# Optimization experiments

Measured on AMD Instinct MI355X. Metric: run time of the kernel, lower is better.

The kernel has to match this reference:

```python
import jax, jax.numpy as jnp
import numpy as np

D = 512      # d_model
H = 8        # n_head
NL = 3       # encoder layers
FF = 2048    # torch TransformerEncoderLayer default dim_feedforward
HID = 256    # hidden_size
ACT = 12     # action_size
NOBJ = 89    # num_objects
BAND = 17    # tril(diagonal=-17) -> keys older than 16 steps banned


def setup_inputs() -> dict:
    key = jax.random.key(0)
    ks = iter(jax.random.split(key, 48))
    rn = lambda shape, s=0.02: jax.random.normal(next(ks), shape, jnp.float32) * s
    b, seq = 16, 512
    inp = {
        'state_input': jax.random.normal(next(ks), (b, seq, 3, 16, 16), jnp.float32),
        'goal_input': jax.random.normal(next(ks), (b, seq, 300), jnp.float32),
        # encoders (stand-ins for obs_enc / lang_enc)
        'W_obs': rn((256, 3 * 16 * 16)), 'b_obs': rn((256,)),
        'W_lang': rn((256, 300)), 'b_lang': rn((256,)),
        # input projection 512 -> 512
        'W_in': rn((D, 512)), 'b_in': rn((D,)),
        # per-layer transformer params, stacked on layer dim
        'Wqkv': rn((NL, 3 * D, D)), 'bqkv': rn((NL, 3 * D)),
        'Wo': rn((NL, D, D)), 'bo': rn((NL, D)),
        'W1': rn((NL, FF, D)), 'b1': rn((NL, FF)),
        'W2': rn((NL, D, FF)), 'b2': rn((NL, D)),
        'g1': jnp.ones((NL, D)), 'bt1': jnp.zeros((NL, D)),
        'g2': jnp.ones((NL, D)), 'bt2': jnp.zeros((NL, D)),
        # output heads
        'W_outp': rn((HID, D)), 'b_outp': rn((HID,)),
        'W_a1': rn((ACT, HID)), 'b_a1': rn((ACT,)),
        'W_a2': rn((NOBJ, HID)), 'b_a2': rn((NOBJ,)),
    }
    return inp


def _ln(y, g, bt):
    m = y.mean(-1, keepdims=True)
    v = y.var(-1, keepdims=True)
    return (y - m) / jnp.sqrt(v + 1e-5) * g + bt


def _encoder(x, mask_add, Wqkv, bqkv, Wo, bo, W1, b1, W2, b2, g1, bt1, g2, bt2):
    b, n, _ = x.shape
    dh = D // H
    scale = 1.0 / np.sqrt(dh)
    for l in range(NL):
        qkv = x @ Wqkv[l].T + bqkv[l]
        q, k, v = jnp.split(qkv, 3, axis=-1)
        hd = lambda t: t.reshape(b, n, H, dh).transpose(0, 2, 1, 3)  # [b,h,n,dh]
        q, k, v = hd(q), hd(k), hd(v)
        sc = jnp.einsum('bhqd,bhkd->bhqk', q, k) * scale + mask_add
        a = jax.nn.softmax(sc, axis=-1)
        o = jnp.einsum('bhqk,bhkd->bhqd', a, v).transpose(0, 2, 1, 3).reshape(b, n, D)
        o = o @ Wo[l].T + bo[l]
        x = _ln(x + o, g1[l], bt1[l])             # post-LN (torch default)
        f = jax.nn.relu(x @ W1[l].T + b1[l]) @ W2[l].T + b2[l]
        x = _ln(x + f, g2[l], bt2[l])
    return x


def reference(state_input, goal_input, W_obs, b_obs, W_lang, b_lang, W_in, b_in,
              Wqkv, bqkv, Wo, bo, W1, b1, W2, b2, g1, bt1, g2, bt2,
              W_outp, b_outp, W_a1, b_a1, W_a2, b_a2):
    b, s = state_input.shape[:2]
    st = state_input.reshape(b, s, -1) @ W_obs.T + b_obs          # obs_enc
    lg = goal_input @ W_lang.T + b_lang                            # lang_enc
    x = jnp.concatenate([st, lg], axis=-1) @ W_in.T + b_in        # [b,s,D]
    # key padding mask; sentinel token appended (causal_mask=False branch)
    pad = ~jnp.any(goal_input != -1, axis=-1)                      # [b,s]
    pad = jnp.concatenate([pad, jnp.zeros((b, 1), bool)], axis=1)
    x = jnp.concatenate([x, jnp.zeros((b, 1, D), x.dtype)], axis=1)
    n = s + 1
    i = jnp.arange(n)
    # banned: tril(-17) | triu(1)  -> attend only to keys in [i-16, i]
    mask2 = ((i[:, None] - i[None, :]) >= BAND) | (i[None, :] > i[:, None])
    banned = mask2[None, None, :, :] | pad[:, None, None, :]
    mask_add = jnp.where(banned, jnp.float32(-1e9), jnp.float32(0.0))
    x = _encoder(x, mask_add, Wqkv, bqkv, Wo, bo, W1, b1, W2, b2, g1, bt1, g2, bt2)
    out = x[:, :-1, :]                                             # drop sentinel
    h = out @ W_outp.T + b_outp
    l1 = h @ W_a1.T + b_a1
    l2 = h @ W_a2.T + b_a2
    return jnp.concatenate([l1, l2], axis=-1)                      # [b,s,101]
```

## Files before the change

kernel.cpp:

```cpp
#include <hip/hip_runtime.h>

#define D 512
#define H 8
#define NL 3
#define FFD 2048
#define HID 256
#define BAND 17
#define BATCH 16
#define SEQ 512
#define MTOK (BATCH * SEQ)
#define NOUT 101
#define NOUTP 128

typedef unsigned short u16;
typedef __attribute__((ext_vector_type(8))) short short8;
typedef __attribute__((ext_vector_type(4))) float f32x4;
typedef __attribute__((ext_vector_type(8))) unsigned short u16x8;

__device__ inline float bf2f(u16 u) {
    union { unsigned int i; float f; } x; x.i = ((unsigned int)u) << 16; return x.f;
}
__device__ inline u16 f2bf(float f) {
    union { float f; unsigned int i; } x; x.f = f;
    unsigned int r = x.i + 0x7fffu + ((x.i >> 16) & 1u);
    return (u16)(r >> 16);
}

__device__ __forceinline__ void gload_lds16(const u16* g, u16* l) {
    __builtin_amdgcn_global_load_lds(
        (const __attribute__((address_space(1))) unsigned int*)(g),
        (__attribute__((address_space(3))) unsigned int*)(l),
        16, 0, 0);
}

#define BM 128
#define BN 128
#define BK 64

__global__ __launch_bounds__(512) void gemm_kernel(
    const u16* __restrict__ A, int lda,
    const u16* __restrict__ B, int ldb,
    const float* __restrict__ bias,
    float* __restrict__ Cf, int ldcf,
    u16* __restrict__ Cb0, u16* __restrict__ Cb1, int ldcb,
    int M, int N, int K, int relu)
{
    __shared__ u16 As[2][BM * BK];
    __shared__ u16 Bs[2][BN * BK];
    const int tid  = threadIdx.x;
    const int lane = tid & 63;
    const int wv   = tid >> 6;
    const int wr = wv >> 2, wc = wv & 3;

    const int nb  = gridDim.x * gridDim.y;
    const int bid = blockIdx.y * gridDim.x + blockIdx.x;
    const int tile = (bid & 7) * (nb >> 3) + (bid >> 3);
    const int m0 = (tile / gridDim.x) * BM;
    const int n0 = (tile % gridDim.x) * BN;
    const int kz = blockIdx.z * K;

    f32x4 acc[4][2] = {};

    const int srow8 = lane >> 3;
    const int schunk = (lane & 7) ^ srow8;
    const size_t aoff0 = (size_t)(m0 + wv * 16 + srow8) * lda + kz + schunk * 8;
    const size_t aoff1 = aoff0 + 8 * lda;
    const size_t boff0 = (size_t)(n0 + wv * 16 + srow8) * ldb + kz + schunk * 8;
    const size_t boff1 = boff0 + 8 * ldb;

    const int frow = lane & 15;
    const int q    = lane >> 4;
    const int rc0 = ((q ^ (frow & 7)) << 3);
    const int rc1 = (((4 + q) ^ (frow & 7)) << 3);

    #define STAGE(buf, k0)                                                    \
        do {                                                                  \
            gload_lds16(A + aoff0 + (k0), &As[buf][(wv * 16 + 0) * BK]);      \
            gload_lds16(A + aoff1 + (k0), &As[buf][(wv * 16 + 8) * BK]);      \
            gload_lds16(B + boff0 + (k0), &Bs[buf][(wv * 16 + 0) * BK]);      \
            gload_lds16(B + boff1 + (k0), &Bs[buf][(wv * 16 + 8) * BK]);      \
        } while (0)

    #define COMPUTE(buf)                                                            \
        do {                                                                        \
            short8 af[4][2], bf[2][2];                                              \
            _Pragma("unroll")                                                       \
            for (int i = 0; i < 4; ++i) {                                           \
                const u16* rp = &As[buf][(wr * 64 + i * 16 + frow) * BK];           \
                af[i][0] = *(const short8*)&rp[rc0];                                \
                af[i][1] = *(const short8*)&rp[rc1];                                \
            }                                                                       \
            _Pragma("unroll")                                                       \
            for (int j = 0; j < 2; ++j) {                                           \
                const u16* rp = &Bs[buf][(wc * 32 + j * 16 + frow) * BK];           \
                bf[j][0] = *(const short8*)&rp[rc0];                                \
                bf[j][1] = *(const short8*)&rp[rc1];                                \
            }                                                                       \
            _Pragma("unroll")                                                       \
            for (int kk = 0; kk < 2; ++kk)                                          \
                _Pragma("unroll")                                                   \
                for (int i = 0; i < 4; ++i)                                         \
                    _Pragma("unroll")                                               \
                    for (int j = 0; j < 2; ++j)                                     \
                        acc[i][j] = __builtin_amdgcn_mfma_f32_16x16x32_bf16(        \
                            af[i][kk], bf[j][kk], acc[i][j], 0, 0, 0);              \
        } while (0)

    const int nt = K >> 6;
    STAGE(0, 0);
    int cur = 0;
    for (int t = 0; t < nt - 1; ++t) {
        STAGE(cur ^ 1, (t + 1) << 6);
        asm volatile("s_waitcnt vmcnt(4)" ::: "memory");
        __builtin_amdgcn_s_barrier();
        __builtin_amdgcn_sched_barrier(0);
        COMPUTE(cur);
        __builtin_amdgcn_s_barrier();
        cur ^= 1;
    }
    asm volatile("s_waitcnt vmcnt(0)" ::: "memory");
    __builtin_amdgcn_s_barrier();
    __builtin_amdgcn_sched_barrier(0);
    COMPUTE(cur);

    #undef STAGE
    #undef COMPUTE

    u16* Cb = blockIdx.z ? Cb1 : Cb0;
    const bool addb = (bias != nullptr) && (blockIdx.z == 0);

    const int crow0 = (lane >> 4) * 4;
    const int ccol  = lane & 15;
    #pragma unroll
    for (int j = 0; j < 2; ++j) {
        int gcol = n0 + wc * 32 + j * 16 + ccol;
        if (gcol >= N) continue;
        float bv = addb ? bias[gcol] : 0.f;
        #pragma unroll
        for (int i = 0; i < 4; ++i) {
            #pragma unroll
            for (int r = 0; r < 4; ++r) {
                int grow = m0 + wr * 64 + i * 16 + crow0 + r;
                float v = acc[i][j][r] + bv;
                if (relu) v = fmaxf(v, 0.f);
                if (Cf) Cf[(size_t)grow * ldcf + gcol] = v;
                if (Cb) Cb[(size_t)grow * ldcb + gcol] = f2bf(v);
            }
        }
    }
}

#define CHUNK 128
#define KSLOT 144
#define VT_LD 152

__global__ __launch_bounds__(512) void attn_kernel(
    const u16* __restrict__ qkv, const unsigned char* __restrict__ pad,
    u16* __restrict__ o)
{
    __shared__ u16 Vt[64 * VT_LD];
    __shared__ u16 Pl[8 * 16 * 40];
    __shared__ unsigned char padl[KSLOT];

    const int tid = threadIdx.x, lane = tid & 63, wv = tid >> 6;
    const int b = blockIdx.z, h = blockIdx.y, c0 = blockIdx.x * CHUNK;
    const u16* base = qkv + (size_t)b * SEQ * (3 * D);

    for (int s = tid; s < KSLOT * 4; s += 512) {
        int t = s >> 2, dq = (s & 3) * 16;
        int j = c0 - 16 + t; if (j < 0) j = 0;
        const u16* vrow = base + (size_t)j * (3 * D) + 2 * D + h * 64 + dq;
        u16 tmp[16];
        *(u16x8*)&tmp[0] = *(const u16x8*)&vrow[0];
        *(u16x8*)&tmp[8] = *(const u16x8*)&vrow[8];
        #pragma unroll
        for (int d = 0; d < 16; ++d)
            Vt[(dq + d) * VT_LD + t] = tmp[d];
    }
    if (tid < KSLOT) {
        int j = c0 - 16 + tid;
        padl[tid] = (j >= 0) ? pad[b * SEQ + j] : (unsigned char)1;
    }
    __syncthreads();

    const int qi0 = wv * 16;
    const int i0  = c0 + qi0;
    const int frow = lane & 15;
    const int g    = lane >> 4;
    const int kg8  = g * 8;
    const int g4   = g * 4;

    short8 qf[2];
    #pragma unroll
    for (int kk = 0; kk < 2; ++kk)
        qf[kk] = *(const short8*)&base[(size_t)(i0 + frow) * (3 * D) + h * 64 + kk * 32 + kg8];

    f32x4 sacc[2] = {};
    #pragma unroll
    for (int jb = 0; jb < 2; ++jb) {
        int jrow = i0 - 16 + jb * 16 + frow; if (jrow < 0) jrow = 0;
        const u16* kbase = base + (size_t)jrow * (3 * D) + D + h * 64;
        #pragma unroll
        for (int kk = 0; kk < 2; ++kk) {
            short8 kf = *(const short8*)&kbase[kk * 32 + kg8];
            sacc[jb] = __builtin_amdgcn_mfma_f32_16x16x32_bf16(qf[kk], kf, sacc[jb], 0, 0, 0);
        }
    }

    float sv[2][4];
    #pragma unroll
    for (int jb = 0; jb < 2; ++jb) {
        int s = jb * 16 + frow;
        int jg = i0 - 16 + s;
        bool padk = (jg < 0) || padl[qi0 + s];
        #pragma unroll
        for (int r = 0; r < 4; ++r) {
            int qq = g4 + r;
            bool banned = (s < qq) || (s > qq + 16) || padk;
            sv[jb][r] = sacc[jb][r] * 0.125f + (banned ? -1e9f : 0.f);
        }
    }

    float ex[2][4], rdn[4];
    #pragma unroll
    for (int r = 0; r < 4; ++r) {
        float m = fmaxf(sv[0][r], sv[1][r]);
        #pragma unroll
        for (int off = 1; off < 16; off <<= 1) m = fmaxf(m, __shfl_xor(m, off));
        float e0 = __expf(sv[0][r] - m);
        float e1 = __expf(sv[1][r] - m);
        float dsum = e0 + e1;
        #pragma unroll
        for (int off = 1; off < 16; off <<= 1) dsum += __shfl_xor(dsum, off);
        ex[0][r] = e0; ex[1][r] = e1;
        rdn[r] = 1.f / dsum;
    }

    u16* Pw = &Pl[wv * 640];
    #pragma unroll
    for (int jb = 0; jb < 2; ++jb)
        #pragma unroll
        for (int r = 0; r < 4; ++r)
            Pw[(g4 + r) * 40 + jb * 16 + frow] = f2bf(ex[jb][r]);
    short8 pa = *(const short8*)&Pw[frow * 40 + kg8];

    f32x4 oacc[4] = {};
    #pragma unroll
    for (int nb = 0; nb < 4; ++nb) {
        short8 vf = *(const short8*)&Vt[(nb * 16 + frow) * VT_LD + qi0 + kg8];
        oacc[nb] = __builtin_amdgcn_mfma_f32_16x16x32_bf16(pa, vf, oacc[nb], 0, 0, 0);
    }

    #pragma unroll
    for (int r = 0; r < 4; ++r) {
        size_t row = (size_t)(b * SEQ + i0 + g4 + r);
        #pragma unroll
        for (int nb = 0; nb < 4; ++nb)
            o[row * D + h * 64 + nb * 16 + frow] = f2bf(oacc[nb][r] * rdn[r]);
    }
}

__global__ __launch_bounds__(256) void resln_kernel(
    const u16* __restrict__ xin,
    const u16* __restrict__ d0, const u16* __restrict__ d1,
    const float* __restrict__ g, const float* __restrict__ bt,
    u16* __restrict__ xb)
{
    int row  = blockIdx.x * 4 + (threadIdx.x >> 6);
    int lane = threadIdx.x & 63;
    u16x8 xv = *(const u16x8*)(xin + (size_t)row * D + lane * 8);
    u16x8 dv0 = *(const u16x8*)(d0 + (size_t)row * D + lane * 8);
    u16x8 dv1 = *(const u16x8*)(d1 + (size_t)row * D + lane * 8);

    float y[8];
    float s = 0.f, s2 = 0.f;
    #pragma unroll
    for (int c = 0; c < 8; ++c) {
        y[c] = bf2f(xv[c]) + bf2f(dv0[c]) + bf2f(dv1[c]);
        s += y[c]; s2 += y[c] * y[c];
    }
    #pragma unroll
    for (int off = 32; off > 0; off >>= 1) {
        s  += __shfl_xor(s, off);
        s2 += __shfl_xor(s2, off);
    }
    float mean = s * (1.f / D);
    float var  = s2 * (1.f / D) - mean * mean;
    float inv  = rsqrtf(fmaxf(var, 0.f) + 1e-5f);

    f32x4 gv0 = ((const f32x4*)g)[lane * 2],  gv1 = ((const f32x4*)g)[lane * 2 + 1];
    f32x4 bv0 = ((const f32x4*)bt)[lane * 2], bv1 = ((const f32x4*)bt)[lane * 2 + 1];
    u16x8 ob;
    #pragma unroll
    for (int c = 0; c < 4; ++c) {
        ob[c]     = f2bf((y[c] - mean) * inv * gv0[c] + bv0[c]);
        ob[c + 4] = f2bf((y[c + 4] - mean) * inv * gv1[c] + bv1[c]);
    }
    *(u16x8*)(xb + (size_t)row * D + lane * 8) = ob;
}

__global__ __launch_bounds__(256) void pad_kernel(
    const float* __restrict__ goal, unsigned char* __restrict__ pad)
{
    int row  = blockIdx.x * 4 + (threadIdx.x >> 6);
    int lane = threadIdx.x & 63;
    const f32x4* gr = (const f32x4*)(goal + (size_t)row * 300);
    bool any = false;
    for (int c4 = lane; c4 < 75; c4 += 64) {
        f32x4 v = gr[c4];
        any |= (v[0] != -1.f) | (v[1] != -1.f) | (v[2] != -1.f) | (v[3] != -1.f);
    }
    unsigned long long b = __ballot(any);
    if (lane == 0) pad[row] = (b == 0ull) ? 1 : 0;
}

struct CvtJob { const float* src; u16* dstb; float* dstf; int n; int mode; };
struct CvtArgs { CvtJob j[15]; int blk0[16]; };

__global__ __launch_bounds__(256) void cvt_kernel(CvtArgs a) {
    const int bx = blockIdx.x;
    int jid = 0;
    #pragma unroll 1
    while (jid < 14 && bx >= a.blk0[jid + 1]) ++jid;
    const CvtJob jb = a.j[jid];
    const int i0 = (bx - a.blk0[jid]) * 2048 + threadIdx.x * 8;
    if (i0 >= jb.n) return;

    if (jb.mode == 0) {
        if (i0 + 8 <= jb.n) {
            f32x4 v0 = *(const f32x4*)(jb.src + i0);
            f32x4 v1 = *(const f32x4*)(jb.src + i0 + 4);
            u16x8 o;
            #pragma unroll
            for (int c = 0; c < 4; ++c) { o[c] = f2bf(v0[c]); o[c + 4] = f2bf(v1[c]); }
            *(u16x8*)(jb.dstb + i0) = o;
        } else {
            for (int e = 0; e < 8 && i0 + e < jb.n; ++e) jb.dstb[i0 + e] = f2bf(jb.src[i0 + e]);
        }
    } else if (jb.mode == 2) {
        int r = (int)((unsigned)i0 / 320u);
        int c = i0 - r * 320;
        const float* s = jb.src + (size_t)r * 300 + c;
        u16x8 o;
        if (c + 8 <= 300) {
            f32x4 v0 = *(const f32x4*)s;
            f32x4 v1 = *(const f32x4*)(s + 4);
            #pragma unroll
            for (int cc = 0; cc < 4; ++cc) { o[cc] = f2bf(v0[cc]); o[cc + 4] = f2bf(v1[cc]); }
        } else {
            #pragma unroll
            for (int e = 0; e < 8; ++e) o[e] = (c + e < 300) ? f2bf(s[e]) : (u16)0;
        }
        *(u16x8*)(jb.dstb + i0) = o;
    } else if (jb.mode == 1) {
        for (int e = 0; e < 8 && i0 + e < jb.n; ++e) jb.dstf[i0 + e] = jb.src[i0 + e];
    } else {
        u16x8 z = {0, 0, 0, 0, 0, 0, 0, 0};
        *(u16x8*)(jb.dstb + i0) = z;
    }
}


extern "C" void kernel_launch(void* const* d_in, const int* in_sizes, int n_in,
                              void* d_out, int out_size, void* d_ws, size_t ws_size,
                              hipStream_t stream)
{
    const float* state  = (const float*)d_in[0];
    const float* goal   = (const float*)d_in[1];
    const float* W_obs  = (const float*)d_in[2];
    const float* b_obs  = (const float*)d_in[3];
    const float* W_lang = (const float*)d_in[4];
    const float* b_lang = (const float*)d_in[5];
    const float* W_in   = (const float*)d_in[6];
    const float* b_in   = (const float*)d_in[7];
    const float* Wqkv   = (const float*)d_in[8];
    const float* bqkv   = (const float*)d_in[9];
    const float* Wo     = (const float*)d_in[10];
    const float* bo     = (const float*)d_in[11];
    const float* W1     = (const float*)d_in[12];
    const float* b1     = (const float*)d_in[13];
    const float* W2     = (const float*)d_in[14];
    const float* b2     = (const float*)d_in[15];
    const float* g1     = (const float*)d_in[16];
    const float* bt1    = (const float*)d_in[17];
    const float* g2     = (const float*)d_in[18];
    const float* bt2    = (const float*)d_in[19];
    const float* W_outp = (const float*)d_in[20];
    const float* b_outp = (const float*)d_in[21];
    const float* W_a1   = (const float*)d_in[22];
    const float* b_a1   = (const float*)d_in[23];
    const float* W_a2   = (const float*)d_in[24];
    const float* b_a2   = (const float*)d_in[25];

    char* ws = (char*)d_ws;
    size_t off = 0;
    auto alloc = [&](size_t bytes) -> void* {
        void* p = ws + off;
        off = (off + bytes + 255) & ~(size_t)255;
        return p;
    };

    u16* wqkv_b  = (u16*)alloc((size_t)NL * 1536 * D * 2);
    u16* wo_b    = (u16*)alloc((size_t)NL * D * D * 2);
    u16* w1_b    = (u16*)alloc((size_t)NL * FFD * D * 2);
    u16* w2_b    = (u16*)alloc((size_t)NL * D * FFD * 2);
    u16* wobs_b  = (u16*)alloc((size_t)256 * 768 * 2);
    u16* wlang_b = (u16*)alloc((size_t)256 * 320 * 2);
    u16* win_b   = (u16*)alloc((size_t)D * D * 2);
    u16* woutp_b = (u16*)alloc((size_t)HID * D * 2);
    u16* wa_b    = (u16*)alloc((size_t)NOUTP * HID * 2);
    float* ba_f  = (float*)alloc((size_t)NOUT * 4);
    u16* state_b = (u16*)alloc((size_t)MTOK * 768 * 2);
    u16* goal_b  = (u16*)alloc((size_t)MTOK * 320 * 2);
    u16* feat_b  = (u16*)alloc((size_t)MTOK * D * 2);
    u16* x_b     = (u16*)alloc((size_t)MTOK * D * 2);
    u16* qkv_b   = (u16*)alloc((size_t)MTOK * 3 * D * 2);
    u16* o_b     = (u16*)alloc((size_t)MTOK * D * 2);
    u16* delta_b = (u16*)alloc((size_t)MTOK * D * 2);
    u16* h1_b    = (u16*)alloc((size_t)MTOK * FFD * 2);
    u16* hout_b  = (u16*)alloc((size_t)MTOK * HID * 2);
    unsigned char* pad_u8 = (unsigned char*)alloc(MTOK);
    u16* delta2_b = state_b;
    (void)ws_size; (void)in_sizes; (void)n_in; (void)out_size;

    CvtArgs ca;
    int nj = 0, blks = 0;
    auto addj = [&](const float* s, u16* db, float* df, int n, int mode) {
        ca.j[nj].src = s; ca.j[nj].dstb = db; ca.j[nj].dstf = df;
        ca.j[nj].n = n; ca.j[nj].mode = mode;
        ca.blk0[nj] = blks;
        blks += (n + 2047) / 2048;
        ++nj;
    };
    addj(state,  state_b, nullptr, MTOK * 768, 0);
    addj(goal,   goal_b,  nullptr, MTOK * 320, 2);
    addj(Wqkv,   wqkv_b,  nullptr, NL * 1536 * D, 0);
    addj(Wo,     wo_b,    nullptr, NL * D * D, 0);
    addj(W1,     w1_b,    nullptr, NL * FFD * D, 0);
    addj(W2,     w2_b,    nullptr, NL * D * FFD, 0);
    addj(W_obs,  wobs_b,  nullptr, 256 * 768, 0);
    addj(W_lang, wlang_b, nullptr, 256 * 320, 2);
    addj(W_in,   win_b,   nullptr, D * D, 0);
    addj(W_outp, woutp_b, nullptr, HID * D, 0);
    addj(W_a1,   wa_b,            nullptr, 12 * HID, 0);
    addj(W_a2,   wa_b + 12 * HID, nullptr, 89 * HID, 0);
    addj(nullptr, wa_b + NOUT * HID, nullptr, (NOUTP - NOUT) * HID, 3);
    addj(b_a1,   nullptr, ba_f,      12, 1);
    addj(b_a2,   nullptr, ba_f + 12, 89, 1);
    ca.blk0[nj] = blks;
    cvt_kernel<<<blks, 256, 0, stream>>>(ca);

    pad_kernel<<<MTOK / 4, 256, 0, stream>>>(goal, pad_u8);

    auto gemm = [&](const u16* A, int lda, const u16* B, int ldb, const float* bias,
                    float* Cf, int ldcf, u16* Cb0, u16* Cb1, int ldcb,
                    int N, int K, int relu, int ksplit) {
        dim3 grid((N + BN - 1) / BN, MTOK / BM, ksplit);
        gemm_kernel<<<grid, 512, 0, stream>>>(A, lda, B, ldb, bias, Cf, ldcf,
                                              Cb0, Cb1, ldcb, MTOK, N, K / ksplit, relu);
    };

    gemm(state_b, 768, wobs_b, 768, b_obs, nullptr, 0, feat_b, nullptr, D, 256, 768, 0, 1);
    gemm(goal_b, 320, wlang_b, 320, b_lang, nullptr, 0, feat_b + 256, nullptr, D, 256, 320, 0, 1);
    gemm(feat_b, D, win_b, D, b_in, nullptr, 0, x_b, nullptr, D, D, D, 0, 1);

    for (int l = 0; l < NL; ++l) {
        gemm(x_b, D, wqkv_b + (size_t)l * 1536 * D, D, bqkv + l * 1536,
             nullptr, 0, qkv_b, nullptr, 3 * D, 3 * D, D, 0, 1);
        {
            dim3 grid(SEQ / CHUNK, H, BATCH);
            attn_kernel<<<grid, 512, 0, stream>>>(qkv_b, pad_u8, o_b);
        }
        gemm(o_b, D, wo_b + (size_t)l * D * D, D, bo + l * D,
             nullptr, 0, delta_b, delta2_b, D, D, D, 0, 2);
        resln_kernel<<<MTOK / 4, 256, 0, stream>>>(x_b, delta_b, delta2_b,
                                                   g1 + l * D, bt1 + l * D, x_b);
        gemm(x_b, D, w1_b + (size_t)l * FFD * D, D, b1 + l * FFD,
             nullptr, 0, h1_b, nullptr, FFD, FFD, D, 1, 1);
        gemm(h1_b, FFD, w2_b + (size_t)l * D * FFD, FFD, b2 + l * D,
             nullptr, 0, delta_b, delta2_b, D, D, FFD, 0, 2);
        resln_kernel<<<MTOK / 4, 256, 0, stream>>>(x_b, delta_b, delta2_b,
                                                   g2 + l * D, bt2 + l * D, x_b);
    }

    gemm(x_b, D, woutp_b, D, b_outp, nullptr, 0, hout_b, nullptr, HID, HID, D, 0, 1);
    gemm(hout_b, HID, wa_b, HID, ba_f, (float*)d_out, NOUT, nullptr, nullptr, 0, NOUT, HID, 0, 1);
}
```

Measured before the change: 369.4 us.

## Fold output projection into action heads as a single fused weight GEMM

Precomputes a combined 128x512 weight (W_a·W_outp) and a combined bias (W_a·b_outp + b_a) on device, then replaces the two final GEMMs (x→hidden 256 and hidden→101) with one GEMM x→101. It removes the intermediate 8192x256 activation write/read and one kernel launch, at the cost of a tiny weight GEMM, a transposing conversion mode and a bias kernel. The GEMM tile swizzle is made conditional so the small weight GEMM with a non-multiple-of-8 block count maps correctly. The fused weight is rounded to bf16 once, which changes rounding slightly compared with the intermediate bf16 hidden activation.

```diff
diff --git a/kernel.cpp b/kernel.cpp
--- a/kernel.cpp
+++ b/kernel.cpp
@@ -54,7 +54,7 @@
 
     const int nb  = gridDim.x * gridDim.y;
     const int bid = blockIdx.y * gridDim.x + blockIdx.x;
-    const int tile = (bid & 7) * (nb >> 3) + (bid >> 3);
+    const int tile = ((nb & 7) == 0) ? ((bid & 7) * (nb >> 3) + (bid >> 3)) : bid;
     const int m0 = (tile / gridDim.x) * BM;
     const int n0 = (tile % gridDim.x) * BN;
     const int kz = blockIdx.z * K;
@@ -312,6 +312,22 @@
     }
     unsigned long long b = __ballot(any);
     if (lane == 0) pad[row] = (b == 0ull) ? 1 : 0;
+}
+
+__global__ __launch_bounds__(128) void headbias_kernel(
+    const float* __restrict__ Wa1, const float* __restrict__ ba1,
+    const float* __restrict__ Wa2, const float* __restrict__ ba2,
+    const float* __restrict__ bout, float* __restrict__ bf)
+{
+    int o = threadIdx.x;
+    float s = 0.f, b = 0.f;
+    const float* wr = nullptr;
+    if (o < 12)       { wr = Wa1 + (size_t)o * HID;        b = ba1[o]; }
+    else if (o < 101) { wr = Wa2 + (size_t)(o - 12) * HID; b = ba2[o - 12]; }
+    if (wr) {
+        for (int h = 0; h < HID; ++h) s += wr[h] * bout[h];
+    }
+    bf[o] = s + b;
 }
 
 struct CvtJob { const float* src; u16* dstb; float* dstf; int n; int mode; };
@@ -351,6 +367,13 @@
             #pragma unroll
             for (int e = 0; e < 8; ++e) o[e] = (c + e < 300) ? f2bf(s[e]) : (u16)0;
         }
+        *(u16x8*)(jb.dstb + i0) = o;
+    } else if (jb.mode == 4) {
+        int j = i0 >> 8;
+        int h = i0 & 255;
+        u16x8 o;
+        #pragma unroll
+        for (int e = 0; e < 8; ++e) o[e] = f2bf(jb.src[(size_t)(h + e) * 512 + j]);
         *(u16x8*)(jb.dstb + i0) = o;
     } else if (jb.mode == 1) {
         for (int e = 0; e < 8 && i0 + e < jb.n; ++e) jb.dstf[i0 + e] = jb.src[i0 + e];
@@ -407,9 +430,10 @@
     u16* wobs_b  = (u16*)alloc((size_t)256 * 768 * 2);
     u16* wlang_b = (u16*)alloc((size_t)256 * 320 * 2);
     u16* win_b   = (u16*)alloc((size_t)D * D * 2);
-    u16* woutp_b = (u16*)alloc((size_t)HID * D * 2);
+    u16* woutpT_b= (u16*)alloc((size_t)D * HID * 2);
     u16* wa_b    = (u16*)alloc((size_t)NOUTP * HID * 2);
-    float* ba_f  = (float*)alloc((size_t)NOUT * 4);
+    u16* wf_b    = (u16*)alloc((size_t)NOUTP * D * 2);
+    float* bf_f  = (float*)alloc((size_t)NOUTP * 4);
     u16* state_b = (u16*)alloc((size_t)MTOK * 768 * 2);
     u16* goal_b  = (u16*)alloc((size_t)MTOK * 320 * 2);
     u16* feat_b  = (u16*)alloc((size_t)MTOK * D * 2);
@@ -418,7 +442,6 @@
     u16* o_b     = (u16*)alloc((size_t)MTOK * D * 2);
     u16* delta_b = (u16*)alloc((size_t)MTOK * D * 2);
     u16* h1_b    = (u16*)alloc((size_t)MTOK * FFD * 2);
-    u16* hout_b  = (u16*)alloc((size_t)MTOK * HID * 2);
     unsigned char* pad_u8 = (unsigned char*)alloc(MTOK);
     u16* delta2_b = state_b;
     (void)ws_size; (void)in_sizes; (void)n_in; (void)out_size;
@@ -441,48 +464,55 @@
     addj(W_obs,  wobs_b,  nullptr, 256 * 768, 0);
     addj(W_lang, wlang_b, nullptr, 256 * 320, 2);
     addj(W_in,   win_b,   nullptr, D * D, 0);
-    addj(W_outp, woutp_b, nullptr, HID * D, 0);
+    addj(W_outp, woutpT_b, nullptr, D * HID, 4);
     addj(W_a1,   wa_b,            nullptr, 12 * HID, 0);
     addj(W_a2,   wa_b + 12 * HID, nullptr, 89 * HID, 0);
     addj(nullptr, wa_b + NOUT * HID, nullptr, (NOUTP - NOUT) * HID, 3);
-    addj(b_a1,   nullptr, ba_f,      12, 1);
-    addj(b_a2,   nullptr, ba_f + 12, 89, 1);
+    addj(b_a1,   nullptr, bf_f,      12, 1);
+    addj(b_a2,   nullptr, bf_f + 12, 89, 1);
     ca.blk0[nj] = blks;
     cvt_kernel<<<blks, 256, 0, stream>>>(ca);
 
     pad_kernel<<<MTOK / 4, 256, 0, stream>>>(goal, pad_u8);
+    headbias_kernel<<<1, 128, 0, stream>>>(W_a1, b_a1, W_a2, b_a2, b_outp, bf_f);
 
     auto gemm = [&](const u16* A, int lda, const u16* B, int ldb, const float* bias,
                     float* Cf, int ldcf, u16* Cb0, u16* Cb1, int ldcb,
-                    int N, int K, int relu, int ksplit) {
-        dim3 grid((N + BN - 1) / BN, MTOK / BM, ksplit);
+                    int M, int N, int K, int relu, int ksplit) {
+        dim3 grid((N + BN - 1) / BN, M / BM, ksplit);
         gemm_kernel<<<grid, 512, 0, stream>>>(A, lda, B, ldb, bias, Cf, ldcf,
-                                              Cb0, Cb1, ldcb, MTOK, N, K / ksplit, relu);
+                                              Cb0, Cb1, ldcb, M, N, K / ksplit, relu);
     };
 
-    gemm(state_b, 768, wobs_b, 768, b_obs, nullptr, 0, feat_b, nullptr, D, 256, 768, 0, 1);
-    gemm(goal_b, 320, wlang_b, 320, b_lang, nullptr, 0, feat_b + 256, nullptr, D, 256, 320, 0, 1);
-    gemm(feat_b, D, win_b, D, b_in, nullptr, 0, x_b, nullptr, D, D, D, 0, 1);
+    gemm(wa_b, HID, woutpT_b, HID, nullptr, nullptr, 0, wf_b, nullptr, D,
+         NOUTP, D, HID, 0, 1);
+
+    gemm(state_b, 768, wobs_b, 768, b_obs, nullptr, 0, feat_b, nullptr, D,
+         MTOK, 256, 768, 0, 1);
+    gemm(goal_b, 320, wlang_b, 320, b_lang, nullptr, 0, feat_b + 256, nullptr, D,
+         MTOK, 256, 320, 0, 1);
+    gemm(feat_b, D, win_b, D, b_in, nullptr, 0, x_b, nullptr, D,
+         MTOK, D, D, 0, 1);
 
     for (int l = 0; l < NL; ++l) {
         gemm(x_b, D, wqkv_b + (size_t)l * 1536 * D, D, bqkv + l * 1536,
-             nullptr, 0, qkv_b, nullptr, 3 * D, 3 * D, D, 0, 1);
+             nullptr, 0, qkv_b, nullptr, 3 * D, MTOK, 3 * D, D, 0, 1);
         {
             dim3 grid(SEQ / CHUNK, H, BATCH);
             attn_kernel<<<grid, 512, 0, stream>>>(qkv_b, pad_u8, o_b);
         }
         gemm(o_b, D, wo_b + (size_t)l * D * D, D, bo + l * D,
-             nullptr, 0, delta_b, delta2_b, D, D, D, 0, 2);
+             nullptr, 0, delta_b, delta2_b, D, MTOK, D, D, 0, 2);
         resln_kernel<<<MTOK / 4, 256, 0, stream>>>(x_b, delta_b, delta2_b,
                                                    g1 + l * D, bt1 + l * D, x_b);
         gemm(x_b, D, w1_b + (size_t)l * FFD * D, D, b1 + l * FFD,
-             nullptr, 0, h1_b, nullptr, FFD, FFD, D, 1, 1);
+             nullptr, 0, h1_b, nullptr, FFD, MTOK, FFD, D, 1, 1);
         gemm(h1_b, FFD, w2_b + (size_t)l * D * FFD, FFD, b2 + l * D,
-             nullptr, 0, delta_b, delta2_b, D, D, FFD, 0, 2);
+             nullptr, 0, delta_b, delta2_b, D, MTOK, D, FFD, 0, 2);
         resln_kernel<<<MTOK / 4, 256, 0, stream>>>(x_b, delta_b, delta2_b,
                                                    g2 + l * D, bt2 + l * D, x_b);
     }
 
-    gemm(x_b, D, woutp_b, D, b_outp, nullptr, 0, hout_b, nullptr, HID, HID, D, 0, 1);
-    gemm(hout_b, HID, wa_b, HID, ba_f, (float*)d_out, NOUT, nullptr, nullptr, 0, NOUT, HID, 0, 1);
-}
+    gemm(x_b, D, wf_b, D, bf_f, (float*)d_out, NOUT, nullptr, nullptr, 0,
+         MTOK, NOUT, D, 0, 1);
+}
```

Result: slower. 377.6 us (+2.2%).
